# Optimization experiments

Hardware: AMD Instinct MI355X
Metric: run time of the kernel (lower is better)

## Reference

```python
import jax, jax.numpy as jnp
import numpy as np

B = 64
D_IN = 4000            # reduced from hardcoded 40000 to fit memory budget (see notes)
N_NODES = 200
ADJ = N_NODES * N_NODES  # 40000 entries per adjacency
E_PER = ADJ // 4         # strictly > 0.75-quantile of 40000 continuous values == top 10000
NEG_SLOPE = 0.2          # GATv2Conv default leaky_relu slope
LN_EPS = 1e-5


def _gelu(x):
    return jax.nn.gelu(x, approximate=False)  # torch F.gelu default = exact erf


def _gatv2(x, src, dst, valid, Wl, bl, Wr, br, att, bias, heads, ch, concat, n):
    # PyG GATv2Conv (share_weights=False): xl = lin_l(x), xr = lin_r(x)
    xl = (x @ Wl + bl).reshape(n, heads, ch)
    xr = (x @ Wr + br).reshape(n, heads, ch)
    e = jax.nn.leaky_relu(xl[src] + xr[dst], NEG_SLOPE)        # [E,H,C]
    logits = jnp.einsum('ehc,hc->eh', e, att)                   # [E,H]
    if valid is not None:
        logits = jnp.where(valid[:, None], logits, -jnp.inf)
    m = jax.ops.segment_max(logits, dst, num_segments=n)
    m = jnp.where(jnp.isfinite(m), m, 0.0)
    ex = jnp.exp(logits - m[dst])
    if valid is not None:
        ex = jnp.where(valid[:, None], ex, 0.0)
    denom = jax.ops.segment_sum(ex, dst, num_segments=n)
    alpha = ex / (denom[dst] + 1e-16)                            # scatter-softmax per target
    out = jax.ops.segment_sum(xl[src] * alpha[..., None], dst, num_segments=n)
    out = out.reshape(n, heads * ch) if concat else out.mean(axis=1)
    return out + bias


def _forward(raw_fc, gbW, gbb, feW1, feb1, feW2, feb2, ln_g, ln_b,
             W1l, b1l, W1r, b1r, att1, bias1,
             W2l, b2l, W2r, b2r, att2, bias2,
             W3l, b3l, W3r, b3r, att3, bias3):
    b = raw_fc.shape[0]
    n = b * N_NODES
    # ---- build_graph ----
    adj = jax.nn.sigmoid(raw_fc @ gbW + gbb).reshape(b, N_NODES, N_NODES)
    adj = (adj + jnp.swapaxes(adj, 1, 2)) * 0.5
    means = adj.mean(axis=2)                    # [B,200]
    stds = jnp.std(adj, axis=2, ddof=1) + 1e-6  # torch std is unbiased
    base = jnp.stack([means, stds], axis=-1).reshape(n, 2)
    h = _gelu(base @ feW1 + feb1) @ feW2 + feb2
    mu = h.mean(-1, keepdims=True)
    var = h.var(-1, keepdims=True)
    x = (h - mu) / jnp.sqrt(var + LN_EPS) * ln_g + ln_b          # LayerNorm(16)
    _, idx = jax.lax.top_k(adj.reshape(b, ADJ), E_PER)           # [B, 10000]
    row = idx // N_NODES
    col = idx % N_NODES
    offs = (jnp.arange(b) * N_NODES)[:, None]
    src = (row + offs).reshape(-1)
    dst = (col + offs).reshape(-1)
    # ---- GAT stack (eval mode: dropout = identity) ----
    x = _gelu(_gatv2(x, src, dst, None, W1l, b1l, W1r, b1r, att1, bias1, 8, 128, True, n))
    # layers 2/3 have add_self_loops=True: remove existing self loops, append one per node
    loops = jnp.arange(n)
    src2 = jnp.concatenate([src, loops])
    dst2 = jnp.concatenate([dst, loops])
    valid2 = jnp.concatenate([src != dst, jnp.ones((n,), bool)])
    x = _gelu(_gatv2(x, src2, dst2, valid2, W2l, b2l, W2r, b2r, att2, bias2, 4, 256, True, n))
    x = _gelu(_gatv2(x, src2, dst2, valid2, W3l, b3l, W3r, b3r, att3, bias3, 1, 512, False, n))
    # global_mean_pool: exactly 200 nodes per graph, contiguous ordering
    return x.reshape(b, N_NODES, 512).mean(axis=1)


def setup_inputs() -> dict:
    key = jax.random.key(0)
    ks = jax.random.split(key, 16)
    f32 = jnp.float32
    def gl(k, shape, fan_in):
        return jax.random.normal(k, shape, f32) / np.sqrt(fan_in)
    inp = {}
    inp['raw_fc'] = jax.random.normal(ks[0], (B, D_IN), f32)
    inp['gbW'] = gl(ks[1], (D_IN, ADJ), D_IN)
    inp['gbb'] = jnp.zeros((ADJ,), f32)
    inp['feW1'] = gl(ks[2], (2, 8), 2);      inp['feb1'] = jnp.zeros((8,), f32)
    inp['feW2'] = gl(ks[3], (8, 16), 8);     inp['feb2'] = jnp.zeros((16,), f32)
    inp['ln_g'] = jnp.ones((16,), f32);      inp['ln_b'] = jnp.zeros((16,), f32)
    inp['W1l'] = gl(ks[4], (16, 8 * 128), 16);   inp['b1l'] = jnp.zeros((8 * 128,), f32)
    inp['W1r'] = gl(ks[5], (16, 8 * 128), 16);   inp['b1r'] = jnp.zeros((8 * 128,), f32)
    inp['att1'] = gl(ks[6], (8, 128), 128);      inp['bias1'] = jnp.zeros((8 * 128,), f32)
    inp['W2l'] = gl(ks[7], (1024, 4 * 256), 1024); inp['b2l'] = jnp.zeros((4 * 256,), f32)
    inp['W2r'] = gl(ks[8], (1024, 4 * 256), 1024); inp['b2r'] = jnp.zeros((4 * 256,), f32)
    inp['att2'] = gl(ks[9], (4, 256), 256);        inp['bias2'] = jnp.zeros((4 * 256,), f32)
    inp['W3l'] = gl(ks[10], (1024, 512), 1024);    inp['b3l'] = jnp.zeros((512,), f32)
    inp['W3r'] = gl(ks[11], (1024, 512), 1024);    inp['b3r'] = jnp.zeros((512,), f32)
    inp['att3'] = gl(ks[12], (1, 512), 512);       inp['bias3'] = jnp.zeros((512,), f32)
    return inp


def reference(raw_fc, gbW, gbb, feW1, feb1, feW2, feb2, ln_g, ln_b,
              W1l, b1l, W1r, b1r, att1, bias1,
              W2l, b2l, W2r, b2r, att2, bias2,
              W3l, b3l, W3r, b3r, att3, bias3):
    return _forward(raw_fc, gbW, gbb, feW1, feb1, feW2, feb2, ln_g, ln_b,
                    W1l, b1l, W1r, b1r, att1, bias1,
                    W2l, b2l, W2r, b2r, att2, bias2,
                    W3l, b3l, W3r, b3r, att3, bias3)
```

## Files before the change

kernel.cpp:

```cpp
#include <hip/hip_runtime.h>
#include <hip/hip_fp16.h>
#include <math.h>
#include <cstdint>
#include <cstddef>

#define NGRAPH 64
#define NN 200
#define ADJN 40000
#define DIN 4000
#define NNODE 12800

typedef float    f32x4 __attribute__((ext_vector_type(4)));
typedef _Float16 f16x8 __attribute__((ext_vector_type(8)));
typedef _Float16 f16x4 __attribute__((ext_vector_type(4)));
typedef _Float16 f16x2 __attribute__((ext_vector_type(2)));
typedef short    bf8v  __attribute__((ext_vector_type(8)));
typedef short    bf4v  __attribute__((ext_vector_type(4)));

union BF8U  { bf8v v; bf4v h[2]; };
union F16X8U{ f16x8 v; f16x4 h[2]; f16x2 p[4]; };

__device__ __forceinline__ unsigned short f2bf(float f) {
  unsigned u = __float_as_uint(f);
  return (unsigned short)((u + 0x7fffu + ((u >> 16) & 1u)) >> 16);
}
__device__ __forceinline__ float bf2f(unsigned short s) {
  return __uint_as_float(((unsigned)s) << 16);
}
__device__ __forceinline__ float gelu_f(float x) {
  return x * 0.5f * (1.0f + erff(x * 0.70710678118654752f));
}

#if defined(__has_builtin)
#if __has_builtin(__builtin_amdgcn_fdot2)
#define FDOT2(a, b, c) __builtin_amdgcn_fdot2((a), (b), (c), false)
#endif
#endif
#ifndef FDOT2
#define FDOT2(a, b, c) ((c) + (float)(a)[0] * (float)(b)[0] + (float)(a)[1] * (float)(b)[1])
#endif

__global__ __launch_bounds__(256) void prep_A(const float* __restrict__ A,
                                              short* __restrict__ Ahi,
                                              short* __restrict__ Alo) {
  const int i = blockIdx.x * 256 + threadIdx.x;
  const float v = A[i];
  const unsigned short h = f2bf(v);
  Ahi[i] = (short)h;
  Alo[i] = (short)f2bf(v - bf2f(h));
}

__global__ __launch_bounds__(256) void transp_all(
    const float* __restrict__ W2l, const float* __restrict__ W2r,
    const float* __restrict__ W3l, const float* __restrict__ W3r,
    _Float16* __restrict__ T2l, _Float16* __restrict__ T2r,
    _Float16* __restrict__ T3l, _Float16* __restrict__ T3r) {
  __shared__ float tile[32][33];
  const int z = blockIdx.z;
  if (z >= 2 && blockIdx.y >= 16) return;
  const float* src = (z == 0) ? W2l : (z == 1) ? W2r : (z == 2) ? W3l : W3r;
  _Float16* dst = (z == 0) ? T2l : (z == 1) ? T2r : (z == 2) ? T3l : T3r;
  const int N = (z < 2) ? 1024 : 512;
  const int K = 1024;
  const int bk = blockIdx.x * 32, bn = blockIdx.y * 32;
  const int tx = threadIdx.x & 31, ty = threadIdx.x >> 5;
#pragma unroll
  for (int r = 0; r < 32; r += 8) tile[ty + r][tx] = src[(size_t)(bk + ty + r) * N + bn + tx];
  __syncthreads();
#pragma unroll
  for (int r = 0; r < 32; r += 8)
    dst[(size_t)(bn + ty + r) * K + bk + tx] = (_Float16)tile[tx][ty + r];
}

#define BA_CONV(PB, W0, W1)                                                     \
  { float wv[8] = {W0.x, W0.y, W0.z, W0.w, W1.x, W1.y, W1.z, W1.w};             \
    _Pragma("unroll") for (int q = 0; q < 8; ++q) {                             \
      unsigned short hh = f2bf(wv[q]);                                          \
      Wh[PB][(wnc + q) * 44 + wk] = (short)hh;                                  \
      Wl[PB][(wnc + q) * 44 + wk] = (short)f2bf(wv[q] - bf2f(hh));              \
    } }

#define BA_MFMA(PB, AHC, ALC)                                                   \
  _Pragma("unroll") for (int j = 0; j < 4; ++j) {                               \
    const int bc = (j * 16 + (lane & 15)) * 44 + kb;                            \
    BF8U bh, bl;                                                                \
    bh.h[0] = *(const bf4v*)(Wh[PB] + bc);                                      \
    bh.h[1] = *(const bf4v*)(Wh[PB] + bc + 4);                                  \
    bl.h[0] = *(const bf4v*)(Wl[PB] + bc);                                      \
    bl.h[1] = *(const bf4v*)(Wl[PB] + bc + 4);                                  \
    acc[j] = __builtin_amdgcn_mfma_f32_16x16x32_bf16(AHC, bh.v, acc[j], 0, 0, 0); \
    acc[j] = __builtin_amdgcn_mfma_f32_16x16x32_bf16(AHC, bl.v, acc[j], 0, 0, 0); \
    acc[j] = __builtin_amdgcn_mfma_f32_16x16x32_bf16(ALC, bh.v, acc[j], 0, 0, 0); \
  }

#define BA_LOADW(W0, W1, K0)                                                    \
  W0 = *(const float4*)(W + (size_t)((K0) + wk) * ADJN + n0 + wnc);             \
  W1 = *(const float4*)(W + (size_t)((K0) + wk) * ADJN + n0 + wnc + 4);

#define BA_LOADA(AH, AL, K0)                                                    \
  AH = *(const bf8v*)(Ahi + (size_t)arow * DIN + (K0) + kb);                    \
  AL = *(const bf8v*)(Alo + (size_t)arow * DIN + (K0) + kb);

__global__ __launch_bounds__(256) void build_adj(
    const short* __restrict__ Ahi, const short* __restrict__ Alo,
    const float* __restrict__ W, const float* __restrict__ bias,
    float* __restrict__ adj) {
  __shared__ short Wh[2][64 * 44], Wl[2][64 * 44];
  const int t = threadIdx.x, wave = t >> 6, lane = t & 63;
  const int n0 = blockIdx.x * 64;
  const int wk = t >> 3, wnc = (t & 7) * 8;
  const int kb = (lane >> 4) * 8;
  const int arow = wave * 16 + (lane & 15);
  f32x4 acc[4] = {};
  float4 w0s0, w1s0, w0s1, w1s1;
  bf8v ahs0, als0, ahs1, als1;
  BA_LOADW(w0s0, w1s0, 0)
  BA_LOADA(ahs0, als0, 0)
  BA_LOADW(w0s1, w1s1, 32)
  BA_LOADA(ahs1, als1, 32)
  BA_CONV(0, w0s0, w1s0)
  for (int it = 0; it < 124; it += 2) {
    __syncthreads();
    {
      const bf8v ahc = ahs0, alc = als0;
      if (it + 2 < 125) {
        const int k2 = (it + 2) * 32;
        BA_LOADW(w0s0, w1s0, k2)
        BA_LOADA(ahs0, als0, k2)
      }
      BA_MFMA(0, ahc, alc)
      BA_CONV(1, w0s1, w1s1)
    }
    __syncthreads();
    {
      const bf8v ahc = ahs1, alc = als1;
      if (it + 3 < 125) {
        const int k2 = (it + 3) * 32;
        BA_LOADW(w0s1, w1s1, k2)
        BA_LOADA(ahs1, als1, k2)
      }
      BA_MFMA(1, ahc, alc)
      if (it + 2 < 125) BA_CONV(0, w0s0, w1s0)
    }
  }
  __syncthreads();
  BA_MFMA(0, ahs0, als0)
#pragma unroll
  for (int j = 0; j < 4; ++j) {
    const int col = n0 + j * 16 + (lane & 15);
    const float bb = bias[col];
#pragma unroll
    for (int vv = 0; vv < 4; ++vv) {
      const int row = wave * 16 + (lane >> 4) * 4 + vv;
      float x = acc[j][vv] + bb;
      adj[(size_t)row * ADJN + col] = 1.0f / (1.0f + __expf(-x));
    }
  }
}

__global__ __launch_bounds__(256) void symmetrize(const float* __restrict__ adj,
                                                  float* __restrict__ adjS) {
  __shared__ float tl[64][65];
  const int g = blockIdx.x;
  const int i0 = (blockIdx.y >> 2) * 64, j0 = (blockIdx.y & 3) * 64;
  const int tx = threadIdx.x & 63, ty = threadIdx.x >> 6;
  const float* ag = adj + (size_t)g * ADJN;
#pragma unroll
  for (int r = 0; r < 64; r += 4) {
    const int jr = j0 + ty + r;
    tl[ty + r][tx] = (jr < NN && i0 + tx < NN) ? ag[jr * NN + i0 + tx] : 0.f;
  }
  __syncthreads();
#pragma unroll
  for (int r = 0; r < 64; r += 4) {
    const int i = i0 + ty + r, j = j0 + tx;
    if (i < NN && j < NN)
      adjS[(size_t)g * ADJN + i * NN + j] = 0.5f * (ag[i * NN + j] + tl[tx][ty + r]);
  }
}

__global__ __launch_bounds__(256) void rowstats(const float* __restrict__ adjS,
                                                float* __restrict__ meanv,
                                                float* __restrict__ stdv) {
  const int row = blockIdx.x * 4 + (threadIdx.x >> 6);
  const int lane = threadIdx.x & 63;
  const float* r = adjS + (size_t)row * NN;
  float s = 0.f, q = 0.f;
#pragma unroll
  for (int k = 0; k < 4; ++k) {
    int i = k * 64 + lane;
    if (i < NN) { float v = r[i]; s += v; q += v * v; }
  }
#pragma unroll
  for (int off = 32; off > 0; off >>= 1) { s += __shfl_xor(s, off); q += __shfl_xor(q, off); }
  if (lane == 0) {
    float m = s * (1.0f / 200.0f);
    float var = (q - 200.0f * m * m) * (1.0f / 199.0f);
    var = fmaxf(var, 0.f);
    meanv[row] = m;
    stdv[row] = sqrtf(var) + 1e-6f;
  }
}

__global__ __launch_bounds__(1024) void radix_lists(
    const float* __restrict__ adjS,
    int* __restrict__ cnt1, int* __restrict__ cnt2,
    unsigned char* __restrict__ list1, unsigned char* __restrict__ list2) {
  __shared__ unsigned hist[4 * 2048];
  __shared__ unsigned s_pref, s_cA;
  const int g = blockIdx.x, t = threadIdx.x, lane = t & 63, wave = t >> 6;
  const float* v = adjS + (size_t)g * ADJN;
  unsigned prefix = 0, pmask = 0, cA = 0;
  const int shifts[3] = {20, 9, 0};
  const int widths[3] = {2048, 2048, 512};
  for (int pass = 0; pass < 3; ++pass) {
    const int nb = widths[pass], sh = shifts[pass];
    for (int i = t; i < 8192; i += 1024) hist[i] = 0u;
    __syncthreads();
    const int cpy = (lane & 3) * 2048;
    for (int e = t; e < ADJN; e += 1024) {
      unsigned u = __float_as_uint(v[e]);
      if ((u & pmask) == prefix) atomicAdd(&hist[cpy + ((u >> sh) & (nb - 1))], 1u);
    }
    __syncthreads();
    if (t < 64) {
      const int CH = nb >> 6;
      unsigned lsum = 0;
      for (int i = 0; i < CH; ++i) {
        const int b = t * CH + i;
        lsum += hist[b] + hist[2048 + b] + hist[4096 + b] + hist[6144 + b];
      }
      unsigned s = lsum;
#pragma unroll
      for (int off = 1; off < 64; off <<= 1) {
        unsigned o = __shfl_down(s, off);
        if (lane + off < 64) s += o;
      }
      const unsigned need = 10000u - cA;
      unsigned sn = __shfl_down(s, 1);
      const unsigned snext = (lane == 63) ? 0u : sn;
      if (s >= need && snext < need) {
        unsigned cum = snext;
        int bsel = t * CH;
        for (int i = CH - 1; i >= 0; --i) {
          const int b = t * CH + i;
          unsigned hb = hist[b] + hist[2048 + b] + hist[4096 + b] + hist[6144 + b];
          if (cum + hb >= need) { bsel = b; break; }
          cum += hb;
        }
        s_pref = prefix | ((unsigned)bsel << sh);
        s_cA = cA + cum;
      }
    }
    __syncthreads();
    prefix = s_pref; cA = s_cA;
    pmask |= (unsigned)(widths[pass] - 1) << sh;
    __syncthreads();
  }
  const float tv = __uint_as_float(prefix);
  for (int j = wave; j < NN; j += 16) {
    const float* row = adjS + (size_t)g * ADJN + (size_t)j * NN;
    unsigned char* l1 = list1 + ((size_t)g * NN + j) * NN;
    unsigned char* l2 = list2 + ((size_t)g * NN + j) * NN;
    int c1 = 0, c2 = 0;
#pragma unroll
    for (int r = 0; r < 4; ++r) {
      int i = r * 64 + lane;
      bool p1 = false, p2 = false;
      if (i < NN) { float vv = row[i]; p1 = (vv >= tv); p2 = p1 && (i != j); }
      unsigned long long b1 = __ballot(p1);
      unsigned long long b2 = __ballot(p2);
      unsigned long long below = (lane == 0) ? 0ull : ((~0ull) >> (64 - lane));
      if (p1) l1[c1 + __popcll(b1 & below)] = (unsigned char)i;
      if (p2) l2[c2 + __popcll(b2 & below)] = (unsigned char)i;
      c1 += (int)__popcll(b1); c2 += (int)__popcll(b2);
    }
    if (lane == 0) {
      l2[c2] = (unsigned char)j;
      cnt1[g * NN + j] = c1;
      cnt2[g * NN + j] = c2 + 1;
    }
  }
}

__global__ __launch_bounds__(256) void lin16_fused(
    const float* __restrict__ meanv, const float* __restrict__ stdv,
    const float* __restrict__ feW1, const float* __restrict__ feb1,
    const float* __restrict__ feW2, const float* __restrict__ feb2,
    const float* __restrict__ ln_g, const float* __restrict__ ln_b,
    const float* __restrict__ Wl, const float* __restrict__ bl,
    const float* __restrict__ Wr, const float* __restrict__ br,
    _Float16* __restrict__ outl, _Float16* __restrict__ outr) {
  __shared__ _Float16 Wt[1024 * 20];
  __shared__ float x0s[16][17];
  const int t = threadIdx.x, wave = t >> 6, lane = t & 63;
  const int mbase = blockIdx.x * 16;
  {
    const int n = t >> 4, o = t & 15;
    const float mu = meanv[mbase + n], sd = stdv[mbase + n];
    float h1[8];
#pragma unroll
    for (int k = 0; k < 8; ++k) h1[k] = gelu_f(mu * feW1[k] + sd * feW1[8 + k] + feb1[k]);
    float h2 = feb2[o];
#pragma unroll
    for (int k = 0; k < 8; ++k) h2 += h1[k] * feW2[k * 16 + o];
    float s = h2;
#pragma unroll
    for (int off = 1; off < 16; off <<= 1) s += __shfl_xor(s, off);
    s *= (1.0f / 16.0f);
    const float d = h2 - s;
    float vv = d * d;
#pragma unroll
    for (int off = 1; off < 16; off <<= 1) vv += __shfl_xor(vv, off);
    vv *= (1.0f / 16.0f);
    x0s[n][o] = d * (1.0f / sqrtf(vv + 1e-5f)) * ln_g[o] + ln_b[o];
  }
  __syncthreads();
  const int mrow = lane & 15, kg = lane >> 4;
  F16X8U af;
#pragma unroll
  for (int q = 0; q < 8; ++q) af.v[q] = (_Float16)0.f;
  if (kg < 2) {
#pragma unroll
    for (int q = 0; q < 8; ++q) af.v[q] = (_Float16)x0s[mrow][kg * 8 + q];
  }
#pragma unroll
  for (int mat = 0; mat < 2; ++mat) {
    if (mat) __syncthreads();
    const float* Wsrc = mat ? Wr : Wl;
    for (int i = t; i < 4096; i += 256) {
      const int k = i >> 8, n4 = (i & 255) * 4;
      float4 wv = *(const float4*)(Wsrc + (size_t)k * 1024 + n4);
      Wt[(n4 + 0) * 20 + k] = (_Float16)wv.x;
      Wt[(n4 + 1) * 20 + k] = (_Float16)wv.y;
      Wt[(n4 + 2) * 20 + k] = (_Float16)wv.z;
      Wt[(n4 + 3) * 20 + k] = (_Float16)wv.w;
    }
    __syncthreads();
    const float* bias = mat ? br : bl;
    _Float16* out = mat ? outr : outl;
#pragma unroll
    for (int nt = 0; nt < 16; ++nt) {
      const int n0 = wave * 256 + nt * 16;
      F16X8U bfv;
#pragma unroll
      for (int q = 0; q < 8; ++q) bfv.v[q] = (_Float16)0.f;
      if (kg < 2) bfv.v = *(const f16x8*)(Wt + (n0 + mrow) * 20 + kg * 8);
      f32x4 acc = {};
      acc = __builtin_amdgcn_mfma_f32_16x16x32_f16(af.v, bfv.v, acc, 0, 0, 0);
      const int col = n0 + mrow;
      const float bb = bias[col];
#pragma unroll
      for (int j = 0; j < 4; ++j)
        out[(size_t)(mbase + kg * 4 + j) * 1024 + col] = (_Float16)(acc[j] + bb);
    }
  }
}

__global__ __launch_bounds__(256, 2) void gemm_nt(
    const _Float16* __restrict__ A,
    const _Float16* __restrict__ Bt0, const _Float16* __restrict__ Bt1,
    const float* __restrict__ b0, const float* __restrict__ b1,
    _Float16* __restrict__ out0, _Float16* __restrict__ out1,
    int Nhalf, int tilesPerHalf) {
  __shared__ _Float16 As[2][128 * 64];
  __shared__ _Float16 Bs[2][128 * 64];
  const int mbase = blockIdx.y * 128;
  const int hsel = blockIdx.x / tilesPerHalf;
  const int ncol0 = (blockIdx.x % tilesPerHalf) * 128;
  const _Float16* Bt = hsel ? Bt1 : Bt0;
  const float* bias = hsel ? b1 : b0;
  _Float16* out = hsel ? out1 : out0;
  const int t = threadIdx.x, wave = t >> 6, lane = t & 63;
  const int wm = wave >> 1, wn = wave & 1;
  f32x4 acc[4][4] = {};
  int crow[4], gco[4], sto[4];
#pragma unroll
  for (int q = 0; q < 4; ++q) {
    const int c = q * 256 + t;
    crow[q] = c >> 3;
    const int sl = c & 7;
    gco[q] = sl * 8;
    sto[q] = crow[q] * 64 + ((sl ^ (crow[q] & 7)) << 3);
  }
  f16x8 ra[4], rb[4];
#pragma unroll
  for (int q = 0; q < 4; ++q) {
    ra[q] = *(const f16x8*)(A + (size_t)(mbase + crow[q]) * 1024 + gco[q]);
    rb[q] = *(const f16x8*)(Bt + (size_t)(ncol0 + crow[q]) * 1024 + gco[q]);
  }
  for (int kt = 0; kt < 16; ++kt) {
    const int p = kt & 1;
#pragma unroll
    for (int q = 0; q < 4; ++q) {
      *(f16x8*)(As[p] + sto[q]) = ra[q];
      *(f16x8*)(Bs[p] + sto[q]) = rb[q];
    }
    __syncthreads();
    if (kt < 15) {
      const int k0 = (kt + 1) * 64;
#pragma unroll
      for (int q = 0; q < 4; ++q) {
        ra[q] = *(const f16x8*)(A + (size_t)(mbase + crow[q]) * 1024 + k0 + gco[q]);
        rb[q] = *(const f16x8*)(Bt + (size_t)(ncol0 + crow[q]) * 1024 + k0 + gco[q]);
      }
    }
#pragma unroll
    for (int ks = 0; ks < 2; ++ks) {
      F16X8U af[4], bfv[4];
#pragma unroll
      for (int m = 0; m < 4; ++m) {
        const int row = wm * 64 + m * 16 + (lane & 15);
        const int kk = ks * 32 + (lane >> 4) * 8;
        af[m].v = *(const f16x8*)(As[p] + row * 64 + (kk ^ ((row & 7) << 3)));
      }
#pragma unroll
      for (int j = 0; j < 4; ++j) {
        const int row = wn * 64 + j * 16 + (lane & 15);
        const int kk = ks * 32 + (lane >> 4) * 8;
        bfv[j].v = *(const f16x8*)(Bs[p] + row * 64 + (kk ^ ((row & 7) << 3)));
      }
#pragma unroll
      for (int j = 0; j < 4; ++j)
#pragma unroll
        for (int m = 0; m < 4; ++m)
          acc[m][j] = __builtin_amdgcn_mfma_f32_16x16x32_f16(af[m].v, bfv[j].v, acc[m][j], 0, 0, 0);
    }
  }
#pragma unroll
  for (int j = 0; j < 4; ++j) {
    const int col = ncol0 + wn * 64 + j * 16 + (lane & 15);
    const float bb = bias[col];
#pragma unroll
    for (int m = 0; m < 4; ++m) {
#pragma unroll
      for (int vv = 0; vv < 4; ++vv) {
        const int row = mbase + wm * 64 + m * 16 + (lane >> 4) * 4 + vv;
        out[(size_t)row * Nhalf + col] = (_Float16)(acc[m][j][vv] + bb);
      }
    }
  }
}

template <int C, int HC, bool USE_LL>
__global__ __launch_bounds__(1024, 4) void gat_layer(
    const _Float16* __restrict__ xlb, const _Float16* __restrict__ xrb,
    const float* __restrict__ attw, const float* __restrict__ biasw,
    const int* __restrict__ cnts, const unsigned char* __restrict__ lists,
    _Float16* __restrict__ outb) {
  extern __shared__ char smem[];
  constexpr int XLB = 200 * C * 2;
  constexpr int XRW = 16 * C * 2;
  _Float16* xr_s = (_Float16*)(smem + XLB);
  _Float16* aw = (_Float16*)(smem + XLB + XRW);
  unsigned char* ll = (unsigned char*)(smem + XLB + XRW + 6400);
  unsigned* att_s = (unsigned*)(smem + XLB + XRW + 6400 + (USE_LL ? 3200 : 0));
  const int g = blockIdx.x;
  const int hd = blockIdx.y;
  const int t = threadIdx.x, wave = t >> 6, lane = t & 63;
  constexpr int GRP = (C == 128) ? 16 : 32;
  constexpr int NG = 64 / GRP;
  const int grp = lane / GRP, li = lane % GRP;

  for (int ch = t; ch < 200 * (C / 8); ch += 1024) {
    const int node = ch / (C / 8), cc = (ch % (C / 8)) * 8;
    f16x8 v = *(const f16x8*)(xlb + (size_t)(g * 200 + node) * HC + hd * C + cc);
    *(f16x8*)(smem + (((node * C + cc) * 2) ^ ((node & 15) << 4))) = v;
  }
  for (int i = t; i < C / 2; i += 1024) {
    f16x2 a;
    a[0] = (_Float16)attw[hd * C + 2 * i];
    a[1] = (_Float16)attw[hd * C + 2 * i + 1];
    att_s[i] = __builtin_bit_cast(unsigned, a);
  }
  __syncthreads();

  _Float16* xr_w = xr_s + wave * C;
  f16x8 xrreg;
  if (lane < C / 8)
    xrreg = *(const f16x8*)(xrb + (size_t)(g * 200 + wave) * HC + hd * C + lane * 8);

  for (int jj = wave; jj < 200; jj += 16) {
    const int gn = g * 200 + jj;
    const int cnt = cnts[gn];
    const unsigned char* lst = lists + (size_t)gn * NN;
    if (lane < C / 8) {
      *(f16x8*)(xr_w + lane * 8) = xrreg;
      if (jj + 16 < 200)
        xrreg = *(const f16x8*)(xrb + (size_t)(gn + 16) * HC + hd * C + lane * 8);
    }
    float lg[4] = {-INFINITY, -INFINITY, -INFINITY, -INFINITY};
#pragma unroll
    for (int r = 0; r < 4; ++r) {
      const int e = (r << 6) + lane;
      if (e < cnt) {
        const int s = lst[e];
        if constexpr (USE_LL) ll[wave * 200 + e] = (unsigned char)s;
        const int swz = (s & 15) << 4;
        float accv[4] = {0.f, 0.f, 0.f, 0.f};
#pragma unroll
        for (int c0 = 0; c0 < C; c0 += 16) {
          const int ai = ((c0 >> 4) & 1) * 2;
          const unsigned* ap = att_s + c0 / 2;
          F16X8U xa, xb, raa, rbb;
          xa.v = *(const f16x8*)(smem + (((s * C + c0) * 2) ^ swz));
          xb.v = *(const f16x8*)(smem + (((s * C + c0 + 8) * 2) ^ swz));
          raa.v = *(const f16x8*)(xr_w + c0);
          rbb.v = *(const f16x8*)(xr_w + c0 + 8);
#pragma unroll
          for (int pq = 0; pq < 4; ++pq) {
            f16x2 z = xa.p[pq] + raa.p[pq];
            f16x2 zs = z * (_Float16)0.2f;
            f16x2 m = __builtin_elementwise_max(z, zs);
            accv[ai] = FDOT2(__builtin_bit_cast(f16x2, ap[pq]), m, accv[ai]);
            f16x2 z2 = xb.p[pq] + rbb.p[pq];
            f16x2 zs2 = z2 * (_Float16)0.2f;
            f16x2 m2 = __builtin_elementwise_max(z2, zs2);
            accv[ai + 1] = FDOT2(__builtin_bit_cast(f16x2, ap[4 + pq]), m2, accv[ai + 1]);
          }
        }
        lg[r] = (accv[0] + accv[1]) + (accv[2] + accv[3]);
      }
    }
    float mloc = fmaxf(fmaxf(lg[0], lg[1]), fmaxf(lg[2], lg[3]));
#pragma unroll
    for (int off = 32; off > 0; off >>= 1) mloc = fmaxf(mloc, __shfl_xor(mloc, off));
    float ex[4]; float ps = 0.f;
#pragma unroll
    for (int r = 0; r < 4; ++r) { ex[r] = __expf(lg[r] - mloc); ps += ex[r]; }
#pragma unroll
    for (int off = 32; off > 0; off >>= 1) ps += __shfl_xor(ps, off);
    const float denom = ps + 1e-16f;
#pragma unroll
    for (int r = 0; r < 4; ++r) {
      const int e = (r << 6) + lane;
      if (e < cnt) aw[wave * 200 + e] = (_Float16)(ex[r] / denom);
    }
    float o[8] = {};
    for (int e0 = 0; e0 < cnt; e0 += NG) {
      const int e = e0 + grp;
      if (e < cnt) {
        const float a = (float)aw[wave * 200 + e];
        int s;
        if constexpr (USE_LL) s = ll[wave * 200 + e]; else s = lst[e];
        const int swz = (s & 15) << 4;
        f16x8 xv = *(const f16x8*)(smem + (((s * C + li * 8) * 2) ^ swz));
#pragma unroll
        for (int q = 0; q < 8; ++q) o[q] += a * (float)xv[q];
      }
    }
#pragma unroll
    for (int q = 0; q < 8; ++q) {
      if constexpr (GRP == 16) o[q] += __shfl_xor(o[q], 16);
      o[q] += __shfl_xor(o[q], 32);
    }
    if (grp == 0) {
      const int colb = hd * C + li * 8;
      f16x8 ov;
#pragma unroll
      for (int q = 0; q < 8; ++q) ov[q] = (_Float16)gelu_f(o[q] + biasw[colb + q]);
      *(f16x8*)(outb + (size_t)gn * HC + colb) = ov;
    }
  }
}

__global__ __launch_bounds__(1024, 4) void gat_l3(
    const _Float16* __restrict__ xlb, const _Float16* __restrict__ xrb,
    const float* __restrict__ attw, const float* __restrict__ biasw,
    const int* __restrict__ cnts, const unsigned char* __restrict__ lists,
    float* __restrict__ psum) {
  extern __shared__ char smem[];
  _Float16* xr_s = (_Float16*)(smem + 51200);
  float* plog = (float*)(smem + 64000);
  unsigned* att_s = (unsigned*)(smem + 104000);
  const int g = blockIdx.x, range = blockIdx.y, r0 = range * 50;
  const int t = threadIdx.x, wave = t >> 6, lane = t & 63;
  const int grp = lane >> 4, li = lane & 15;

  for (int chunk = 0; chunk < 4; ++chunk) {
    if (chunk) __syncthreads();
    for (int ch = t; ch < 200 * 16; ch += 1024) {
      const int node = ch >> 4, cc = (ch & 15) * 8;
      *(f16x8*)(smem + (((node * 128 + cc) * 2) ^ ((node & 15) << 4))) =
          *(const f16x8*)(xlb + (size_t)(g * 200 + node) * 512 + chunk * 128 + cc);
    }
    for (int ch = t; ch < 50 * 16; ch += 1024) {
      const int node = ch >> 4, cc = (ch & 15) * 8;
      *(f16x8*)(xr_s + node * 128 + cc) =
          *(const f16x8*)(xrb + (size_t)(g * 200 + r0 + node) * 512 + chunk * 128 + cc);
    }
    for (int i = t; i < 64; i += 1024) {
      f16x2 a;
      a[0] = (_Float16)attw[chunk * 128 + 2 * i];
      a[1] = (_Float16)attw[chunk * 128 + 2 * i + 1];
      att_s[i] = __builtin_bit_cast(unsigned, a);
    }
    __syncthreads();
    for (int jj = wave; jj < 50; jj += 16) {
      const int gn = g * 200 + r0 + jj;
      const int cnt = cnts[gn];
      const unsigned char* lst = lists + (size_t)gn * NN;
#pragma unroll
      for (int r = 0; r < 4; ++r) {
        const int e = (r << 6) + lane;
        if (e < cnt) {
          const int s = lst[e];
          const int swz = (s & 15) << 4;
          float accv[4] = {0.f, 0.f, 0.f, 0.f};
#pragma unroll
          for (int c0 = 0; c0 < 128; c0 += 16) {
            const int ai = ((c0 >> 4) & 1) * 2;
            const unsigned* ap = att_s + c0 / 2;
            F16X8U xa, xb, raa, rbb;
            xa.v = *(const f16x8*)(smem + (((s * 128 + c0) * 2) ^ swz));
            xb.v = *(const f16x8*)(smem + (((s * 128 + c0 + 8) * 2) ^ swz));
            raa.v = *(const f16x8*)(xr_s + jj * 128 + c0);
            rbb.v = *(const f16x8*)(xr_s + jj * 128 + c0 + 8);
#pragma unroll
            for (int pq = 0; pq < 4; ++pq) {
              f16x2 z = xa.p[pq] + raa.p[pq];
              f16x2 zs = z * (_Float16)0.2f;
              f16x2 m = __builtin_elementwise_max(z, zs);
              accv[ai] = FDOT2(__builtin_bit_cast(f16x2, ap[pq]), m, accv[ai]);
              f16x2 z2 = xb.p[pq] + rbb.p[pq];
              f16x2 zs2 = z2 * (_Float16)0.2f;
              f16x2 m2 = __builtin_elementwise_max(z2, zs2);
              accv[ai + 1] = FDOT2(__builtin_bit_cast(f16x2, ap[4 + pq]), m2, accv[ai + 1]);
            }
          }
          const float acc = (accv[0] + accv[1]) + (accv[2] + accv[3]);
          if (chunk == 0) plog[jj * 200 + e] = acc;
          else plog[jj * 200 + e] += acc;
        }
      }
    }
  }
  __syncthreads();
  for (int jj = wave; jj < 50; jj += 16) {
    const int gn = g * 200 + r0 + jj;
    const int cnt = cnts[gn];
    float lg[4] = {-INFINITY, -INFINITY, -INFINITY, -INFINITY};
#pragma unroll
    for (int r = 0; r < 4; ++r) {
      const int e = (r << 6) + lane;
      if (e < cnt) lg[r] = plog[jj * 200 + e];
    }
    float mloc = fmaxf(fmaxf(lg[0], lg[1]), fmaxf(lg[2], lg[3]));
#pragma unroll
    for (int off = 32; off > 0; off >>= 1) mloc = fmaxf(mloc, __shfl_xor(mloc, off));
    float ex[4]; float ps = 0.f;
#pragma unroll
    for (int r = 0; r < 4; ++r) { ex[r] = __expf(lg[r] - mloc); ps += ex[r]; }
#pragma unroll
    for (int off = 32; off > 0; off >>= 1) ps += __shfl_xor(ps, off);
    const float denom = ps + 1e-16f;
#pragma unroll
    for (int r = 0; r < 4; ++r) {
      const int e = (r << 6) + lane;
      if (e < cnt) plog[jj * 200 + e] = ex[r] / denom;
    }
  }
  for (int chunk = 0; chunk < 4; ++chunk) {
    __syncthreads();
    for (int ch = t; ch < 200 * 16; ch += 1024) {
      const int node = ch >> 4, cc = (ch & 15) * 8;
      *(f16x8*)(smem + (((node * 128 + cc) * 2) ^ ((node & 15) << 4))) =
          *(const f16x8*)(xlb + (size_t)(g * 200 + node) * 512 + chunk * 128 + cc);
    }
    __syncthreads();
    float p[8] = {};
    for (int jj = wave; jj < 50; jj += 16) {
      const int gn = g * 200 + r0 + jj;
      const int cnt = cnts[gn];
      const unsigned char* lst = lists + (size_t)gn * NN;
      float o[8] = {};
      for (int e0 = 0; e0 < cnt; e0 += 4) {
        const int e = e0 + grp;
        if (e < cnt) {
          const float a = plog[jj * 200 + e];
          const int s = lst[e];
          const int swz = (s & 15) << 4;
          f16x8 xv = *(const f16x8*)(smem + (((s * 128 + li * 8) * 2) ^ swz));
#pragma unroll
          for (int q = 0; q < 8; ++q) o[q] += a * (float)xv[q];
        }
      }
#pragma unroll
      for (int q = 0; q < 8; ++q) {
        o[q] += __shfl_xor(o[q], 16);
        o[q] += __shfl_xor(o[q], 32);
      }
      if (grp == 0) {
        const int colb = chunk * 128 + li * 8;
#pragma unroll
        for (int q = 0; q < 8; ++q) p[q] += gelu_f(o[q] + biasw[colb + q]);
      }
    }
    if (grp == 0) {
      const int slot = range * 16 + wave;
      float* pd = psum + ((size_t)slot * 64 + g) * 512 + chunk * 128 + li * 8;
      float4 a0 = {p[0], p[1], p[2], p[3]};
      float4 a1 = {p[4], p[5], p[6], p[7]};
      *(float4*)pd = a0;
      *(float4*)(pd + 4) = a1;
    }
  }
}

__global__ void finalize(const float* __restrict__ psum, float* __restrict__ out) {
  const int idx = blockIdx.x * 256 + threadIdx.x;
  float s = 0.f;
#pragma unroll
  for (int k = 0; k < 64; ++k) s += psum[(size_t)k * 32768 + idx];
  out[idx] = s * 0.005f;
}

extern "C" void kernel_launch(void* const* d_in, const int* in_sizes, int n_in,
                              void* d_out, int out_size, void* d_ws, size_t ws_size,
                              hipStream_t stream) {
  const float* raw_fc = (const float*)d_in[0];
  const float* gbW = (const float*)d_in[1];
  const float* gbb = (const float*)d_in[2];
  const float* feW1 = (const float*)d_in[3];
  const float* feb1 = (const float*)d_in[4];
  const float* feW2 = (const float*)d_in[5];
  const float* feb2 = (const float*)d_in[6];
  const float* ln_g = (const float*)d_in[7];
  const float* ln_b = (const float*)d_in[8];
  const float* W1l = (const float*)d_in[9];  const float* b1l = (const float*)d_in[10];
  const float* W1r = (const float*)d_in[11]; const float* b1r = (const float*)d_in[12];
  const float* att1 = (const float*)d_in[13]; const float* bias1 = (const float*)d_in[14];
  const float* W2l = (const float*)d_in[15]; const float* b2l = (const float*)d_in[16];
  const float* W2r = (const float*)d_in[17]; const float* b2r = (const float*)d_in[18];
  const float* att2 = (const float*)d_in[19]; const float* bias2 = (const float*)d_in[20];
  const float* W3l = (const float*)d_in[21]; const float* b3l = (const float*)d_in[22];
  const float* W3r = (const float*)d_in[23]; const float* b3r = (const float*)d_in[24];
  const float* att3 = (const float*)d_in[25]; const float* bias3 = (const float*)d_in[26];

  if (ws_size < 121000000) return;

  char* w = (char*)d_ws;
  float* adj   = (float*)(w + 0);
  float* adjS  = (float*)(w + 10240000);
  float* meanv = (float*)(w + 20480000);
  float* stdv  = (float*)(w + 20531200);
  int* cnt1    = (int*)(w + 21401856);
  int* cnt2    = (int*)(w + 21453056);
  unsigned char* list1 = (unsigned char*)(w + 21504256);
  unsigned char* list2 = (unsigned char*)(w + 24064256);
  _Float16* bufA = (_Float16*)(w + 26624256);
  _Float16* bufB = (_Float16*)(w + 52838656);
  _Float16* bufC = (_Float16*)(w + 79053056);
  float* psum = (float*)(w + 105267456);
  short* Ahi  = (short*)(w + 113656064);
  short* Alo  = (short*)(w + 114168064);
  _Float16* Wt2l = (_Float16*)(w + 114680064);
  _Float16* Wt2r = (_Float16*)(w + 116777216);
  _Float16* Wt3l = (_Float16*)(w + 118874368);
  _Float16* Wt3r = (_Float16*)(w + 119922944);

  const int SMEM_L1 = 65152;
  const int SMEM_L2 = 117504;
  const int SMEM_L3 = 104256;
  hipFuncSetAttribute((const void*)gat_layer<128, 1024, true>,
                      hipFuncAttributeMaxDynamicSharedMemorySize, SMEM_L1);
  hipFuncSetAttribute((const void*)gat_layer<256, 1024, false>,
                      hipFuncAttributeMaxDynamicSharedMemorySize, SMEM_L2);
  hipFuncSetAttribute((const void*)gat_l3,
                      hipFuncAttributeMaxDynamicSharedMemorySize, SMEM_L3);

  prep_A<<<1000, 256, 0, stream>>>(raw_fc, Ahi, Alo);
  transp_all<<<dim3(32, 32, 4), 256, 0, stream>>>(W2l, W2r, W3l, W3r, Wt2l, Wt2r, Wt3l, Wt3r);
  build_adj<<<625, 256, 0, stream>>>(Ahi, Alo, gbW, gbb, adj);
  symmetrize<<<dim3(64, 16), 256, 0, stream>>>(adj, adjS);
  rowstats<<<3200, 256, 0, stream>>>(adjS, meanv, stdv);
  radix_lists<<<64, 1024, 0, stream>>>(adjS, cnt1, cnt2, list1, list2);
  lin16_fused<<<800, 256, 0, stream>>>(meanv, stdv, feW1, feb1, feW2, feb2, ln_g, ln_b,
                                       W1l, b1l, W1r, b1r, bufA, bufB);
  gat_layer<128, 1024, true><<<dim3(64, 8), 1024, SMEM_L1, stream>>>(
      bufA, bufB, att1, bias1, cnt1, list1, bufC);
  gemm_nt<<<dim3(16, 100), 256, 0, stream>>>(bufC, Wt2l, Wt2r, b2l, b2r, bufA, bufB, 1024, 8);
  gat_layer<256, 1024, false><<<dim3(64, 4), 1024, SMEM_L2, stream>>>(
      bufA, bufB, att2, bias2, cnt2, list2, bufC);
  gemm_nt<<<dim3(8, 100), 256, 0, stream>>>(bufC, Wt3l, Wt3r, b3l, b3r, bufA, bufB, 512, 4);
  gat_l3<<<dim3(64, 4), 1024, SMEM_L3, stream>>>(bufA, bufB, att3, bias3, cnt2, list2, psum);
  finalize<<<128, 256, 0, stream>>>(psum, (float*)d_out);
}
```

Measured before the change: 976.7 us.

## Use direct global-to-LDS loads in gemm_nt and vectorize W staging in build_adj

Result: no change. 968.9 us (-0.8%).

```diff
diff --git a/kernel.cpp b/kernel.cpp
--- a/kernel.cpp
+++ b/kernel.cpp
@@ -39,6 +39,12 @@
 #ifndef FDOT2
 #define FDOT2(a, b, c) ((c) + (float)(a)[0] * (float)(b)[0] + (float)(a)[1] * (float)(b)[1])
 #endif
+
+__device__ __forceinline__ void glds16(const _Float16* g, _Float16* l) {
+  __builtin_amdgcn_global_load_lds(
+      (const __attribute__((address_space(1))) void*)g,
+      (__attribute__((address_space(3))) void*)l, 16, 0, 0);
+}
 
 __global__ __launch_bounds__(256) void prep_A(const float* __restrict__ A,
                                               short* __restrict__ Ahi,
@@ -72,13 +78,27 @@
     dst[(size_t)(bn + ty + r) * K + bk + tx] = (_Float16)tile[tx][ty + r];
 }
 
-#define BA_CONV(PB, W0, W1)                                                     \
-  { float wv[8] = {W0.x, W0.y, W0.z, W0.w, W1.x, W1.y, W1.z, W1.w};             \
-    _Pragma("unroll") for (int q = 0; q < 8; ++q) {                             \
-      unsigned short hh = f2bf(wv[q]);                                          \
-      Wh[PB][(wnc + q) * 44 + wk] = (short)hh;                                  \
-      Wl[PB][(wnc + q) * 44 + wk] = (short)f2bf(wv[q] - bf2f(hh));              \
-    } }
+#define BA_LOADW(WV, K0)                                                        \
+  _Pragma("unroll") for (int q = 0; q < 8; ++q)                                 \
+    WV[q] = W[(size_t)((K0) + kgrp * 8 + q) * ADJN + n0 + nn];
+
+#define BA_CONV(PB, WV)                                                         \
+  { bf4v h0, h1, l0, l1;                                                        \
+    _Pragma("unroll") for (int i = 0; i < 4; ++i) {                             \
+      unsigned short hh = (unsigned short)(__float_as_uint(WV[i]) >> 16);       \
+      h0[i] = (short)hh;                                                        \
+      l0[i] = (short)f2bf(WV[i] - bf2f(hh));                                    \
+    }                                                                           \
+    _Pragma("unroll") for (int i = 0; i < 4; ++i) {                             \
+      unsigned short hh = (unsigned short)(__float_as_uint(WV[4 + i]) >> 16);   \
+      h1[i] = (short)hh;                                                        \
+      l1[i] = (short)f2bf(WV[4 + i] - bf2f(hh));                                \
+    }                                                                           \
+    *(bf4v*)(Wh[PB] + nn * 44 + kgrp * 8)     = h0;                             \
+    *(bf4v*)(Wh[PB] + nn * 44 + kgrp * 8 + 4) = h1;                             \
+    *(bf4v*)(Wl[PB] + nn * 44 + kgrp * 8)     = l0;                             \
+    *(bf4v*)(Wl[PB] + nn * 44 + kgrp * 8 + 4) = l1;                             \
+  }
 
 #define BA_MFMA(PB, AHC, ALC)                                                   \
   _Pragma("unroll") for (int j = 0; j < 4; ++j) {                               \
@@ -93,10 +113,6 @@
     acc[j] = __builtin_amdgcn_mfma_f32_16x16x32_bf16(ALC, bh.v, acc[j], 0, 0, 0); \
   }
 
-#define BA_LOADW(W0, W1, K0)                                                    \
-  W0 = *(const float4*)(W + (size_t)((K0) + wk) * ADJN + n0 + wnc);             \
-  W1 = *(const float4*)(W + (size_t)((K0) + wk) * ADJN + n0 + wnc + 4);
-
 #define BA_LOADA(AH, AL, K0)                                                    \
   AH = *(const bf8v*)(Ahi + (size_t)arow * DIN + (K0) + kb);                    \
   AL = *(const bf8v*)(Alo + (size_t)arow * DIN + (K0) + kb);
@@ -108,39 +124,39 @@
   __shared__ short Wh[2][64 * 44], Wl[2][64 * 44];
   const int t = threadIdx.x, wave = t >> 6, lane = t & 63;
   const int n0 = blockIdx.x * 64;
-  const int wk = t >> 3, wnc = (t & 7) * 8;
+  const int nn = t & 63, kgrp = t >> 6;
   const int kb = (lane >> 4) * 8;
   const int arow = wave * 16 + (lane & 15);
   f32x4 acc[4] = {};
-  float4 w0s0, w1s0, w0s1, w1s1;
+  float wva[8], wvb[8];
   bf8v ahs0, als0, ahs1, als1;
-  BA_LOADW(w0s0, w1s0, 0)
+  BA_LOADW(wva, 0)
   BA_LOADA(ahs0, als0, 0)
-  BA_LOADW(w0s1, w1s1, 32)
+  BA_LOADW(wvb, 32)
   BA_LOADA(ahs1, als1, 32)
-  BA_CONV(0, w0s0, w1s0)
+  BA_CONV(0, wva)
   for (int it = 0; it < 124; it += 2) {
     __syncthreads();
     {
       const bf8v ahc = ahs0, alc = als0;
       if (it + 2 < 125) {
         const int k2 = (it + 2) * 32;
-        BA_LOADW(w0s0, w1s0, k2)
+        BA_LOADW(wva, k2)
         BA_LOADA(ahs0, als0, k2)
       }
       BA_MFMA(0, ahc, alc)
-      BA_CONV(1, w0s1, w1s1)
+      BA_CONV(1, wvb)
     }
     __syncthreads();
     {
       const bf8v ahc = ahs1, alc = als1;
       if (it + 3 < 125) {
         const int k2 = (it + 3) * 32;
-        BA_LOADW(w0s1, w1s1, k2)
+        BA_LOADW(wvb, k2)
         BA_LOADA(ahs1, als1, k2)
       }
       BA_MFMA(1, ahc, alc)
-      if (it + 2 < 125) BA_CONV(0, w0s0, w1s0)
+      if (it + 2 < 125) BA_CONV(0, wva)
     }
   }
   __syncthreads();
@@ -374,35 +390,24 @@
   const int t = threadIdx.x, wave = t >> 6, lane = t & 63;
   const int wm = wave >> 1, wn = wave & 1;
   f32x4 acc[4][4] = {};
-  int crow[4], gco[4], sto[4];
-#pragma unroll
-  for (int q = 0; q < 4; ++q) {
-    const int c = q * 256 + t;
-    crow[q] = c >> 3;
-    const int sl = c & 7;
-    gco[q] = sl * 8;
-    sto[q] = crow[q] * 64 + ((sl ^ (crow[q] & 7)) << 3);
-  }
-  f16x8 ra[4], rb[4];
-#pragma unroll
-  for (int q = 0; q < 4; ++q) {
-    ra[q] = *(const f16x8*)(A + (size_t)(mbase + crow[q]) * 1024 + gco[q]);
-    rb[q] = *(const f16x8*)(Bt + (size_t)(ncol0 + crow[q]) * 1024 + gco[q]);
-  }
+  const int srow = lane >> 3;
+  const int sg = (lane & 7) ^ srow;
+#pragma unroll
+  for (int c = 0; c < 4; ++c) {
+    const int rbase = wave * 32 + c * 8;
+    glds16(A + (size_t)(mbase + rbase + srow) * 1024 + sg * 8, As[0] + rbase * 64);
+    glds16(Bt + (size_t)(ncol0 + rbase + srow) * 1024 + sg * 8, Bs[0] + rbase * 64);
+  }
+  __syncthreads();
   for (int kt = 0; kt < 16; ++kt) {
     const int p = kt & 1;
-#pragma unroll
-    for (int q = 0; q < 4; ++q) {
-      *(f16x8*)(As[p] + sto[q]) = ra[q];
-      *(f16x8*)(Bs[p] + sto[q]) = rb[q];
-    }
-    __syncthreads();
     if (kt < 15) {
       const int k0 = (kt + 1) * 64;
 #pragma unroll
-      for (int q = 0; q < 4; ++q) {
-        ra[q] = *(const f16x8*)(A + (size_t)(mbase + crow[q]) * 1024 + k0 + gco[q]);
-        rb[q] = *(const f16x8*)(Bt + (size_t)(ncol0 + crow[q]) * 1024 + k0 + gco[q]);
+      for (int c = 0; c < 4; ++c) {
+        const int rbase = wave * 32 + c * 8;
+        glds16(A + (size_t)(mbase + rbase + srow) * 1024 + k0 + sg * 8, As[p ^ 1] + rbase * 64);
+        glds16(Bt + (size_t)(ncol0 + rbase + srow) * 1024 + k0 + sg * 8, Bs[p ^ 1] + rbase * 64);
       }
     }
 #pragma unroll
@@ -426,6 +431,7 @@
         for (int m = 0; m < 4; ++m)
           acc[m][j] = __builtin_amdgcn_mfma_f32_16x16x32_f16(af[m].v, bfv[j].v, acc[m][j], 0, 0, 0);
     }
+    __syncthreads();
   }
 #pragma unroll
   for (int j = 0; j < 4; ++j) {
```
